# Performance work log

Measured on AMD Instinct MI355X. Metric: run time of the kernel, lower is better.

The kernel has to match this reference:

```python
import jax, jax.numpy as jnp
import numpy as np

DIM, H, K, RADIUS = 128, 4, 32, 0.3
DH = DIM // H
N, M = 16384, 4096


def setup_inputs() -> dict:
    key = jax.random.key(0)
    ks = jax.random.split(key, 16)
    s = 0.02
    return {
        "xyz": jax.random.normal(ks[0], (N, 3), jnp.float32),
        "feats": jax.random.normal(ks[1], (N, DIM), jnp.float32),
        "idx_center": jax.random.randint(ks[2], (M,), 0, N, jnp.int64),
        "Wq": jax.random.normal(ks[3], (DIM, DIM), jnp.float32) * s,
        "Wk": jax.random.normal(ks[4], (DIM, DIM), jnp.float32) * s,
        "Wv": jax.random.normal(ks[5], (DIM, DIM), jnp.float32) * s,
        "Wo": jax.random.normal(ks[6], (DIM, DIM), jnp.float32) * s,
        "bo": jnp.zeros((DIM,), jnp.float32),
        "g1": jnp.ones((DIM,), jnp.float32),
        "be1": jnp.zeros((DIM,), jnp.float32),
        "g2": jnp.ones((DIM,), jnp.float32),
        "be2": jnp.zeros((DIM,), jnp.float32),
        "W1": jax.random.normal(ks[7], (4 * DIM, DIM), jnp.float32) * s,
        "b1f": jnp.zeros((4 * DIM,), jnp.float32),
        "W2": jax.random.normal(ks[8], (DIM, 4 * DIM), jnp.float32) * s,
        "b2f": jnp.zeros((DIM,), jnp.float32),
    }


def _layernorm(x, g, b, eps=1e-5):
    mu = x.mean(-1, keepdims=True)
    var = ((x - mu) ** 2).mean(-1, keepdims=True)
    return (x - mu) / jnp.sqrt(var + eps) * g + b


def reference(xyz, feats, idx_center, Wq, Wk, Wv, Wo, bo, g1, be1, g2, be2, W1, b1f, W2, b2f):
    m = idx_center.shape[0]
    c_xyz = xyz[idx_center]          # (M,3)
    c_feat = feats[idx_center]       # (M,DIM)
    # pairwise Euclidean distance (M,N), like torch.cdist
    d2 = (jnp.sum(c_xyz * c_xyz, -1)[:, None] + jnp.sum(xyz * xyz, -1)[None, :]
          - 2.0 * (c_xyz @ xyz.T))
    dist = jnp.sqrt(jnp.maximum(d2, 1e-12))
    mask = dist < RADIUS
    mask = mask.at[jnp.arange(m), idx_center].set(True)  # force self-inclusion
    dmask = jnp.where(mask, dist, jnp.inf)
    neg_d, nbr_idx = jax.lax.top_k(-dmask, K)            # k smallest distances
    nbr_dist = -neg_d
    valid = jnp.isfinite(nbr_dist)                       # (M,K)
    nbr_feats = jnp.where(valid[..., None], feats[nbr_idx], 0.0)  # (M,K,DIM)
    # tiny per-center attention
    q = (c_feat @ Wq.T).reshape(m, H, DH)
    k = (nbr_feats @ Wk.T).reshape(m, K, H, DH).transpose(0, 2, 1, 3)  # (M,H,K,DH)
    v = (nbr_feats @ Wv.T).reshape(m, K, H, DH).transpose(0, 2, 1, 3)
    attn = jnp.einsum('mhd,mhkd->mhk', q * (DH ** -0.5), k)
    attn = jnp.where(valid[:, None, :], attn, -1e9)
    attn = jax.nn.softmax(attn, axis=-1)
    out = jnp.einsum('mhk,mhkd->mhd', attn, v)
    out = out.transpose(0, 2, 1).reshape(m, DIM)  # matches torch transpose(1,2).reshape
    upd = out @ Wo.T + bo
    c_feat = c_feat + _layernorm(upd, g1, be1)
    ffn = jax.nn.relu(c_feat @ W1.T + b1f) @ W2.T + b2f
    c_feat = c_feat + _layernorm(ffn, g2, be2)
    nearest = jnp.argmin(dist, axis=0)            # (N,) nearest center per point
    return feats + c_feat[nearest]
```

## Files before the change

kernel.cpp:

```cpp
#include <hip/hip_runtime.h>
#include <hip/hip_bf16.h>

#define DIMF 128
#define KNBR 32
#define NH 4
#define DH 32
#define RADIUS 0.3f
#define CB 8
#define CAND 256
#define PPB 32

#define PACK_BLOCKS 172

typedef unsigned long long u64t;
typedef _Float16 f16x8 __attribute__((ext_vector_type(8)));
typedef _Float16 f16x4 __attribute__((ext_vector_type(4)));
typedef float f32x4 __attribute__((ext_vector_type(4)));

__device__ __forceinline__ void tr4_tile(const float4* __restrict__ in4, float4* __restrict__ out4,
                                         int AI, int BI, int a0, int b0, int t, char* smem) {
    float4(*tile)[33] = (float4(*)[33])smem;
    int tx = t & 31, ty = t >> 5;
    for (int r = ty; r < 32; r += 8) tile[r][tx] = in4[(long)(b0 + r) * AI + a0 + tx];
    __syncthreads();
    for (int r = ty; r < 32; r += 8) out4[(long)(a0 + r) * BI + b0 + tx] = tile[tx][r];
}

__global__ __launch_bounds__(256) void pack_kernel(
    const float* __restrict__ xyz, const int* __restrict__ idxc,
    const float* __restrict__ Wq, const float* __restrict__ Wv,
    const float* __restrict__ Wo, const float* __restrict__ W1,
    const float* __restrict__ W2, const float* __restrict__ Wk,
    float4* __restrict__ qp4, float4* __restrict__ vp4, float4* __restrict__ op4,
    float4* __restrict__ kp4, f16x8* __restrict__ w1h, f16x8* __restrict__ w2h,
    float4* __restrict__ xyz4, float4* __restrict__ cds4, int N, int M) {
    __shared__ __align__(16) char smem[16896];
    int pk = blockIdx.x, t = threadIdx.x;
    if (pk < 4) {
        tr4_tile((const float4*)Wq, qp4, 32, 128, 0, pk * 32, t, smem);
    } else if (pk < 8) {
        tr4_tile((const float4*)Wv, vp4, 32, 128, 0, (pk - 4) * 32, t, smem);
    } else if (pk < 12) {
        tr4_tile((const float4*)Wo, op4, 32, 128, 0, (pk - 8) * 32, t, smem);
    } else if (pk < 28) {
        int idx = (pk - 12) * 256 + t;
        int q = idx >> 7, j = idx & 127;
        float4 w;
        w.x = Wk[(long)(4 * q + 0) * DIMF + j];
        w.y = Wk[(long)(4 * q + 1) * DIMF + j];
        w.z = Wk[(long)(4 * q + 2) * DIMF + j];
        w.w = Wk[(long)(4 * q + 3) * DIMF + j];
        kp4[q * DIMF + j] = w;
    } else if (pk < 92) {
        int idx = (pk - 28) * 256 + t;
        if (idx < N) {
            float x = xyz[3 * idx], y = xyz[3 * idx + 1], z = xyz[3 * idx + 2];
            xyz4[idx] = make_float4(x, y, z, (x * x + y * y) + z * z);
        }
    } else if (pk < 108) {
        int idx = (pk - 92) * 256 + t;
        if (idx < M) {
            int ic = idxc[idx];
            float cx = xyz[3 * ic], cy = xyz[3 * ic + 1], cz = xyz[3 * ic + 2];
            cds4[idx] = make_float4(-2.0f * cx, -2.0f * cy, -2.0f * cz,
                                    (cx * cx + cy * cy) + cz * cz);
        }
    } else if (pk < 140) {
        int e = (pk - 108) * 256 + t;
        int l = e & 63, ks = (e >> 6) & 3, nt = e >> 8;
        int row = nt * 16 + (l & 15);
        int cb = ks * 32 + (l >> 4) * 8;
        const float* src = W1 + (long)row * DIMF + cb;
        f16x8 v;
#pragma unroll
        for (int j = 0; j < 8; ++j) v[j] = (_Float16)src[j];
        w1h[e] = v;
    } else {
        int e = (pk - 140) * 256 + t;
        int l = e & 63, ks = (e >> 6) & 15, nt = e >> 10;
        int row = nt * 16 + (l & 15);
        int cb = ks * 32 + (l >> 4) * 8;
        const float* src = W2 + (long)row * (4 * DIMF) + cb;
        f16x8 v;
#pragma unroll
        for (int j = 0; j < 8; ++j) v[j] = (_Float16)src[j];
        w2h[e] = v;
    }
}

__global__ __launch_bounds__(256) void main_kernel(
    const float4* __restrict__ xyz4, const float4* __restrict__ cds4g,
    const float* __restrict__ feats, const int* __restrict__ idxc,
    const float4* __restrict__ qp4, const float4* __restrict__ kp4,
    const float4* __restrict__ vp4, const float4* __restrict__ op4,
    const float* __restrict__ bo, const float* __restrict__ g1,
    const float* __restrict__ be1, const float* __restrict__ g2,
    const float* __restrict__ be2, const f16x8* __restrict__ w1h,
    const float* __restrict__ b1f, const f16x8* __restrict__ w2h,
    const float* __restrict__ b2f, float* __restrict__ cfin,
    int* __restrict__ bestm, int N, int M) {
    __shared__ __align__(16) char smem[32768];
    __shared__ int nbrl[CB][KNBR];
    __shared__ int cnt[CB];

    int t = threadIdx.x;
    int b = blockIdx.x;
    int nAttn = M / CB;

    if (b >= nAttn) {
        float4* cds = (float4*)smem;
        int pt = t >> 3, q = t & 7;
        int n = (b - nAttn) * PPB + pt;
        float4 p4 = xyz4[n];
        float px = p4.x, py = p4.y, pz = p4.z;
        float bd0 = INFINITY, bd1 = INFINITY;
        int bm0 = 0, bm1 = 0;
        for (int c0 = 0; c0 < M; c0 += 1024) {
            __syncthreads();
            for (int i = t; i < 1024; i += 256) cds[i] = cds4g[c0 + i];
            __syncthreads();
#pragma unroll 8
            for (int i = 0; i < 64; ++i) {
                int ci0 = q + (2 * i) * 8, ci1 = q + (2 * i + 1) * 8;
                float4 ca = cds[ci0];
                float4 cb = cds[ci1];
                float sa = fmaf(ca.x, px, fmaf(ca.y, py, fmaf(ca.z, pz, ca.w)));
                float sb = fmaf(cb.x, px, fmaf(cb.y, py, fmaf(cb.z, pz, cb.w)));
                if (sa < bd0) { bd0 = sa; bm0 = c0 + ci0; }
                if (sb < bd1) { bd1 = sb; bm1 = c0 + ci1; }
            }
        }
        if (bd1 < bd0 || (bd1 == bd0 && bm1 < bm0)) { bd0 = bd1; bm0 = bm1; }
#pragma unroll
        for (int o = 1; o < 8; o <<= 1) {
            float obd = __shfl_xor(bd0, o);
            int obm = __shfl_xor(bm0, o);
            if (obd < bd0 || (obd == bd0 && obm < bm0)) { bd0 = obd; bm0 = obm; }
        }
        if (q == 0) bestm[n] = bm0;
        return;
    }

    int m0 = b * CB;

    {
        u64t(*cand)[CAND] = (u64t(*)[CAND])smem;
        if (t < CB) cnt[t] = 0;
        __syncthreads();
        float nx[CB], ny[CB], nz[CB], cw[CB];
#pragma unroll
        for (int tc = 0; tc < CB; ++tc) {
            float4 c4v = cds4g[m0 + tc];
            nx[tc] = c4v.x; ny[tc] = c4v.y; nz[tc] = c4v.z; cw[tc] = c4v.w;
        }
        const float R2 = RADIUS * RADIUS;
        for (int n = t; n < N; n += 256) {
            float4 p4 = xyz4[n];
            float rhs = R2 - p4.w;
#pragma unroll
            for (int tc = 0; tc < CB; ++tc) {
                float s = fmaf(nx[tc], p4.x, fmaf(ny[tc], p4.y, fmaf(nz[tc], p4.z, cw[tc])));
                if (s < rhs) {
                    int pos = atomicAdd(&cnt[tc], 1);
                    if (pos < CAND)
                        cand[tc][pos] = (((u64t)__float_as_uint(fmaxf(s + p4.w, 0.0f))) << 32) | (unsigned)n;
                }
            }
        }
        __syncthreads();
        int w = t >> 6, lane = t & 63;
        for (int rep = 0; rep < 2; ++rep) {
            int cidx = w + rep * 4;
            int C = cnt[cidx] < CAND ? cnt[cidx] : CAND;
            const u64t* vc = cand[cidx];
            if (C <= 64) {
                u64t mykey = (lane < C) ? vc[lane] : ~0ull;
                int rank = 0;
                for (int j = 0; j < C; ++j) rank += (vc[j] < mykey) ? 1 : 0;
                if (lane < C && rank < KNBR) nbrl[cidx][rank] = (int)(mykey & 0xffffffffu);
                if (lane >= C && lane < KNBR) nbrl[cidx][lane] = -1;
            } else {
                u64t mykey[4];
                int myrank[4];
#pragma unroll
                for (int s = 0; s < 4; ++s) {
                    int i = s * 64 + lane;
                    mykey[s] = (i < C) ? vc[i] : ~0ull;
                    myrank[s] = 0;
                }
                for (int j = 0; j < C; ++j) {
                    u64t kj = vc[j];
#pragma unroll
                    for (int s = 0; s < 4; ++s) myrank[s] += (kj < mykey[s]) ? 1 : 0;
                }
#pragma unroll
                for (int s = 0; s < 4; ++s) {
                    int i = s * 64 + lane;
                    if (i < C && myrank[s] < KNBR) nbrl[cidx][myrank[s]] = (int)(mykey[s] & 0xffffffffu);
                }
            }
        }
    }
    __syncthreads();

    float(*cf)[DIMF] = (float(*)[DIMF])smem;
    float(*cf2)[DIMF] = (float(*)[DIMF])(smem + 4096);
    float(*S1)[4 * DIMF] = (float(*)[4 * DIMF])(smem + 8192);
    float(*S2)[DIMF] = (float(*)[DIMF])(smem + 24576);
    float(*S3)[DIMF] = (float(*)[DIMF])(smem + 28672);

    int lane127 = t & 127;
    int cg = (t >> 7) * 4;
    int c8 = t >> 5, k32 = t & 31;

    {
        int ic = idxc[m0 + c8];
        *(float4*)&cf[c8][k32 * 4] = *(const float4*)&feats[(long)ic * DIMF + k32 * 4];
    }
    __syncthreads();

    {
        float acc[4] = {0.f, 0.f, 0.f, 0.f};
        for (int jj = 0; jj < 32; ++jj) {
            float4 w = qp4[jj * DIMF + lane127];
#pragma unroll
            for (int cc = 0; cc < 4; ++cc) {
                float4 x = *(const float4*)&cf[cg + cc][jj * 4];
                acc[cc] += w.x * x.x + w.y * x.y + w.z * x.z + w.w * x.w;
            }
        }
#pragma unroll
        for (int cc = 0; cc < 4; ++cc) S2[cg + cc][lane127] = acc[cc] * 0.17677669529663687f;
    }
    __syncthreads();

    {
        int j = lane127, hs = t >> 7;
#pragma unroll
        for (int hh = 0; hh < 2; ++hh) {
            int h = hs * 2 + hh;
            float acc[8] = {0.f, 0.f, 0.f, 0.f, 0.f, 0.f, 0.f, 0.f};
            for (int d4 = 0; d4 < 8; ++d4) {
                float4 w = kp4[(h * 8 + d4) * DIMF + j];
#pragma unroll
                for (int c = 0; c < 8; ++c) {
                    float4 qv = *(const float4*)&S2[c][h * DH + d4 * 4];
                    acc[c] += qv.x * w.x + qv.y * w.y + qv.z * w.z + qv.w * w.w;
                }
            }
#pragma unroll
            for (int c = 0; c < 8; ++c) S1[c][h * DIMF + j] = acc[c];
        }
    }
    __syncthreads();

    {
        int ni = nbrl[c8][k32];
        const float* nrow = feats + (long)(ni < 0 ? 0 : ni) * DIMF;
        float lg[4] = {0.f, 0.f, 0.f, 0.f};
        for (int jj = 0; jj < 32; ++jj) {
            float4 f = *(const float4*)&nrow[jj * 4];
#pragma unroll
            for (int h = 0; h < 4; ++h) {
                float4 qwv = *(const float4*)&S1[c8][h * DIMF + jj * 4];
                lg[h] += f.x * qwv.x + f.y * qwv.y + f.z * qwv.z + f.w * qwv.w;
            }
        }
        if (ni < 0) { lg[0] = -1e9f; lg[1] = -1e9f; lg[2] = -1e9f; lg[3] = -1e9f; }
#pragma unroll
        for (int h = 0; h < 4; ++h) {
            float mx = lg[h];
            for (int o = 16; o; o >>= 1) mx = fmaxf(mx, __shfl_xor(mx, o, 32));
            float e = expf(lg[h] - mx);
            float s = e;
            for (int o = 16; o; o >>= 1) s += __shfl_xor(s, o, 32);
            S3[c8][h * KNBR + k32] = e / s;
        }
    }
    __syncthreads();

    {
        int j4 = k32 * 4;
        float a0x = 0.f, a0y = 0.f, a0z = 0.f, a0w = 0.f;
        float a1x = 0.f, a1y = 0.f, a1z = 0.f, a1w = 0.f;
        float a2x = 0.f, a2y = 0.f, a2z = 0.f, a2w = 0.f;
        float a3x = 0.f, a3y = 0.f, a3z = 0.f, a3w = 0.f;
        for (int k = 0; k < KNBR; ++k) {
            int ni = nbrl[c8][k];
            const float* nrow = feats + (long)(ni < 0 ? 0 : ni) * DIMF;
            float4 f = *(const float4*)&nrow[j4];
            float w0 = S3[c8][0 * KNBR + k], w1 = S3[c8][1 * KNBR + k];
            float w2 = S3[c8][2 * KNBR + k], w3 = S3[c8][3 * KNBR + k];
            a0x += w0 * f.x; a0y += w0 * f.y; a0z += w0 * f.z; a0w += w0 * f.w;
            a1x += w1 * f.x; a1y += w1 * f.y; a1z += w1 * f.z; a1w += w1 * f.w;
            a2x += w2 * f.x; a2y += w2 * f.y; a2z += w2 * f.z; a2w += w2 * f.w;
            a3x += w3 * f.x; a3y += w3 * f.y; a3z += w3 * f.z; a3w += w3 * f.w;
        }
        __syncthreads();
        *(float4*)&S1[c8][0 * DIMF + j4] = make_float4(a0x, a0y, a0z, a0w);
        *(float4*)&S1[c8][1 * DIMF + j4] = make_float4(a1x, a1y, a1z, a1w);
        *(float4*)&S1[c8][2 * DIMF + j4] = make_float4(a2x, a2y, a2z, a2w);
        *(float4*)&S1[c8][3 * DIMF + j4] = make_float4(a3x, a3y, a3z, a3w);
    }
    __syncthreads();

    {
        int i = lane127, h = i >> 5, d = i & 31;
        float acc[4] = {0.f, 0.f, 0.f, 0.f};
        for (int jj = 0; jj < 32; ++jj) {
            float4 w = vp4[jj * DIMF + i];
#pragma unroll
            for (int cc = 0; cc < 4; ++cc) {
                float4 pv = *(const float4*)&S1[cg + cc][h * DIMF + jj * 4];
                acc[cc] += w.x * pv.x + w.y * pv.y + w.z * pv.z + w.w * pv.w;
            }
        }
        __syncthreads();
#pragma unroll
        for (int cc = 0; cc < 4; ++cc) S2[cg + cc][d * NH + h] = acc[cc];
    }
    __syncthreads();

    {
        int i = lane127;
        float acc[4] = {0.f, 0.f, 0.f, 0.f};
        for (int jj = 0; jj < 32; ++jj) {
            float4 w = op4[jj * DIMF + i];
#pragma unroll
            for (int cc = 0; cc < 4; ++cc) {
                float4 x = *(const float4*)&S2[cg + cc][jj * 4];
                acc[cc] += w.x * x.x + w.y * x.y + w.z * x.z + w.w * x.w;
            }
        }
        float b = bo[i];
        __syncthreads();
#pragma unroll
        for (int cc = 0; cc < 4; ++cc) S3[cg + cc][i] = acc[cc] + b;
    }
    __syncthreads();

    {
        int i4 = k32 * 4;
        float4 u = *(const float4*)&S3[c8][i4];
        float s = ((u.x + u.y) + u.z) + u.w;
        for (int o = 16; o; o >>= 1) s += __shfl_xor(s, o, 32);
        float mu = s * (1.0f / DIMF);
        float d0 = u.x - mu, d1 = u.y - mu, d2 = u.z - mu, d3 = u.w - mu;
        float vs = ((d0 * d0 + d1 * d1) + d2 * d2) + d3 * d3;
        for (int o = 16; o; o >>= 1) vs += __shfl_xor(vs, o, 32);
        float rs = 1.0f / sqrtf(vs * (1.0f / DIMF) + 1e-5f);
        float4 g = *(const float4*)&g1[i4];
        float4 b = *(const float4*)&be1[i4];
        float4 base = *(const float4*)&cf[c8][i4];
        float4 r;
        r.x = base.x + d0 * rs * g.x + b.x;
        r.y = base.y + d1 * rs * g.y + b.y;
        r.z = base.z + d2 * rs * g.z + b.z;
        r.w = base.w + d3 * rs * g.w + b.w;
        *(float4*)&cf2[c8][i4] = r;
        {
            int byteoff = (c8 * 256 + i4 * 2) ^ ((c8 & 7) << 4);
            f16x4 hv = {(_Float16)r.x, (_Float16)r.y, (_Float16)r.z, (_Float16)r.w};
            *(f16x4*)(smem + 24576 + byteoff) = hv;
        }
    }
    __syncthreads();

    {
        int lane = t & 63, w = t >> 6;
        int la = lane & 15, kg = lane >> 4;
        f16x8 afr[4];
#pragma unroll
        for (int ks = 0; ks < 4; ++ks) {
            int byteoff = (la * 256 + ks * 64 + kg * 16) ^ ((la & 7) << 4);
            afr[ks] = *(const f16x8*)(smem + 24576 + byteoff);
        }
#pragma unroll
        for (int nt0 = 0; nt0 < 8; ++nt0) {
            int nt = w * 8 + nt0;
            f32x4 acc = {0.f, 0.f, 0.f, 0.f};
#pragma unroll
            for (int ks = 0; ks < 4; ++ks) {
                f16x8 bfr = w1h[(nt * 4 + ks) * 64 + lane];
                acc = __builtin_amdgcn_mfma_f32_16x16x32_f16(afr[ks], bfr, acc, 0, 0, 0);
            }
            int col = nt * 16 + la;
            float bb = b1f[col];
#pragma unroll
            for (int r = 0; r < 4; ++r) {
                int row = kg * 4 + r;
                float v = fmaxf(acc[r] + bb, 0.f);
                int byteoff = (row * 1024 + col * 2) ^ ((row & 7) << 4);
                *(_Float16*)(smem + 8192 + byteoff) = (_Float16)v;
            }
        }
    }
    __syncthreads();

    {
        int lane = t & 63, w = t >> 6;
        int la = lane & 15, kg = lane >> 4;
        int nt0 = w * 2, nt1 = w * 2 + 1;
        f32x4 acc0 = {0.f, 0.f, 0.f, 0.f}, acc1 = {0.f, 0.f, 0.f, 0.f};
#pragma unroll
        for (int ks = 0; ks < 16; ++ks) {
            int byteoff = (la * 1024 + ks * 64 + kg * 16) ^ ((la & 7) << 4);
            f16x8 afr = *(const f16x8*)(smem + 8192 + byteoff);
            f16x8 b0 = w2h[(nt0 * 16 + ks) * 64 + lane];
            f16x8 b1v = w2h[(nt1 * 16 + ks) * 64 + lane];
            acc0 = __builtin_amdgcn_mfma_f32_16x16x32_f16(afr, b0, acc0, 0, 0, 0);
            acc1 = __builtin_amdgcn_mfma_f32_16x16x32_f16(afr, b1v, acc1, 0, 0, 0);
        }
        if (lane < 32) {
            float bb0 = b2f[nt0 * 16 + la];
            float bb1 = b2f[nt1 * 16 + la];
#pragma unroll
            for (int r = 0; r < 4; ++r) {
                int row = kg * 4 + r;
                S3[row][nt0 * 16 + la] = acc0[r] + bb0;
                S3[row][nt1 * 16 + la] = acc1[r] + bb1;
            }
        }
    }
    __syncthreads();

    {
        int i4 = k32 * 4;
        float4 u = *(const float4*)&S3[c8][i4];
        float s = ((u.x + u.y) + u.z) + u.w;
        for (int o = 16; o; o >>= 1) s += __shfl_xor(s, o, 32);
        float mu = s * (1.0f / DIMF);
        float d0 = u.x - mu, d1 = u.y - mu, d2 = u.z - mu, d3 = u.w - mu;
        float vs = ((d0 * d0 + d1 * d1) + d2 * d2) + d3 * d3;
        for (int o = 16; o; o >>= 1) vs += __shfl_xor(vs, o, 32);
        float rs = 1.0f / sqrtf(vs * (1.0f / DIMF) + 1e-5f);
        float4 g = *(const float4*)&g2[i4];
        float4 b = *(const float4*)&be2[i4];
        float4 base = *(const float4*)&cf2[c8][i4];
        float4 r;
        r.x = base.x + d0 * rs * g.x + b.x;
        r.y = base.y + d1 * rs * g.y + b.y;
        r.z = base.z + d2 * rs * g.z + b.z;
        r.w = base.w + d3 * rs * g.w + b.w;
        *(float4*)&cfin[(long)(m0 + c8) * DIMF + i4] = r;
    }
}

__global__ __launch_bounds__(256) void out_kernel(const float4* __restrict__ feats4,
                                                  const float* __restrict__ cfin,
                                                  const int* __restrict__ bestm,
                                                  float4* __restrict__ out4, int total) {
    int idx = blockIdx.x * 256 + threadIdx.x;
    if (idx >= total) return;
    int n = idx >> 5, c = idx & 31;
    const float4* cf4 = (const float4*)cfin;
    float4 f = feats4[idx];
    float4 g = cf4[(long)bestm[n] * 32 + c];
    out4[idx] = make_float4(f.x + g.x, f.y + g.y, f.z + g.z, f.w + g.w);
}

extern "C" void kernel_launch(void* const* d_in, const int* in_sizes, int n_in,
                              void* d_out, int out_size, void* d_ws, size_t ws_size,
                              hipStream_t stream) {
    const float* xyz = (const float*)d_in[0];
    const float* feats = (const float*)d_in[1];
    const int* idxc = (const int*)d_in[2];
    const float* Wq = (const float*)d_in[3];
    const float* Wk = (const float*)d_in[4];
    const float* Wv = (const float*)d_in[5];
    const float* Wo = (const float*)d_in[6];
    const float* bo = (const float*)d_in[7];
    const float* g1 = (const float*)d_in[8];
    const float* be1 = (const float*)d_in[9];
    const float* g2 = (const float*)d_in[10];
    const float* be2 = (const float*)d_in[11];
    const float* W1 = (const float*)d_in[12];
    const float* b1f = (const float*)d_in[13];
    const float* W2 = (const float*)d_in[14];
    const float* b2f = (const float*)d_in[15];

    int N = in_sizes[0] / 3;
    int M = in_sizes[2];

    char* ws = (char*)d_ws;
    size_t off = 0;
    float* cfin = (float*)(ws + off); off += (size_t)M * DIMF * 4;
    int* bestm = (int*)(ws + off); off += (size_t)N * 4;
    float4* qp4 = (float4*)(ws + off); off += (size_t)DIMF * DIMF * 4;
    float4* vp4 = (float4*)(ws + off); off += (size_t)DIMF * DIMF * 4;
    float4* op4 = (float4*)(ws + off); off += (size_t)DIMF * DIMF * 4;
    float4* kp4 = (float4*)(ws + off); off += (size_t)DIMF * DIMF * 4;
    f16x8* w1h = (f16x8*)(ws + off); off += (size_t)8192 * 16;
    f16x8* w2h = (f16x8*)(ws + off); off += (size_t)8192 * 16;
    float4* xyz4 = (float4*)(ws + off); off += (size_t)N * 16;
    float4* cds4 = (float4*)(ws + off); off += (size_t)M * 16;
    (void)ws_size; (void)n_in; (void)out_size;

    pack_kernel<<<PACK_BLOCKS, 256, 0, stream>>>(
        xyz, idxc, Wq, Wv, Wo, W1, W2, Wk,
        qp4, vp4, op4, kp4, w1h, w2h, xyz4, cds4, N, M);
    main_kernel<<<M / CB + N / PPB, 256, 0, stream>>>(
        xyz4, cds4, feats, idxc, qp4, kp4, vp4, op4, bo, g1, be1, g2, be2,
        w1h, b1f, w2h, b2f, cfin, bestm, N, M);
    out_kernel<<<(N * DIMF / 4 + 255) / 256, 256, 0, stream>>>(
        (const float4*)feats, cfin, bestm, (float4*)d_out, N * DIMF / 4);
}
```

Measured before the change: 167.9 us.

## Assign two centers per wavefront to remove block barriers in attention stages

Restructures the attention part of the main kernel so each 64-lane wavefront owns two centers end to end, with private shared-memory regions for q, q·Wk, softmax weights and the Wv/Wo stages. This removes most of the __syncthreads between the per-center stages. In exchange, each wave reloads the Wq/Wk/Wv/Wo weights itself, so global/L2 weight traffic grows up to fourfold per block. Shared memory grows from 32 KB to 52 KB, which may reduce occupancy.

```diff
diff --git a/kernel.cpp b/kernel.cpp
--- a/kernel.cpp
+++ b/kernel.cpp
@@ -99,7 +99,7 @@
     const float* __restrict__ b1f, const f16x8* __restrict__ w2h,
     const float* __restrict__ b2f, float* __restrict__ cfin,
     int* __restrict__ bestm, int N, int M) {
-    __shared__ __align__(16) char smem[32768];
+    __shared__ __align__(16) char smem[53248];
     __shared__ int nbrl[CB][KNBR];
     __shared__ int cnt[CB];
 
@@ -168,9 +168,9 @@
             }
         }
         __syncthreads();
-        int w = t >> 6, lane = t & 63;
+        int wv = t >> 6, lane = t & 63;
         for (int rep = 0; rep < 2; ++rep) {
-            int cidx = w + rep * 4;
+            int cidx = wv + rep * 4;
             int C = cnt[cidx] < CAND ? cnt[cidx] : CAND;
             const u64t* vc = cand[cidx];
             if (C <= 64) {
@@ -203,145 +203,139 @@
     }
     __syncthreads();
 
-    float(*cf)[DIMF] = (float(*)[DIMF])smem;
-    float(*cf2)[DIMF] = (float(*)[DIMF])(smem + 4096);
-    float(*S1)[4 * DIMF] = (float(*)[4 * DIMF])(smem + 8192);
-    float(*S2)[DIMF] = (float(*)[DIMF])(smem + 24576);
-    float(*S3)[DIMF] = (float(*)[DIMF])(smem + 28672);
-
-    int lane127 = t & 127;
-    int cg = (t >> 7) * 4;
-    int c8 = t >> 5, k32 = t & 31;
-
-    {
-        int ic = idxc[m0 + c8];
-        *(float4*)&cf[c8][k32 * 4] = *(const float4*)&feats[(long)ic * DIMF + k32 * 4];
-    }
-    __syncthreads();
-
-    {
-        float acc[4] = {0.f, 0.f, 0.f, 0.f};
+    int w = t >> 6, lane = t & 63;
+    float* qwp = (float*)(smem) + w * 1024;
+    float* cfw = (float*)(smem + 16384) + w * 256;
+    float* qb = (float*)(smem + 20480) + w * 256;
+    float* smu = (float*)(smem + 24576) + w * 256;
+    float* cf2w = (float*)(smem + 28672) + w * 256;
+    float* S3out = (float*)(smem + 16384);
+
+    int cl = lane >> 5, l31 = lane & 31;
+    int crow = 2 * w + cl;
+
+    {
+        int ic = idxc[m0 + crow];
+        *(float4*)(cfw + cl * 128 + l31 * 4) = *(const float4*)&feats[(long)ic * DIMF + l31 * 4];
+    }
+
+#pragma unroll
+    for (int c = 0; c < 2; ++c) {
+        float acc0 = 0.f, acc1 = 0.f;
+        const float4* cf4 = (const float4*)(cfw + c * 128);
         for (int jj = 0; jj < 32; ++jj) {
-            float4 w = qp4[jj * DIMF + lane127];
-#pragma unroll
-            for (int cc = 0; cc < 4; ++cc) {
-                float4 x = *(const float4*)&cf[cg + cc][jj * 4];
-                acc[cc] += w.x * x.x + w.y * x.y + w.z * x.z + w.w * x.w;
-            }
-        }
-#pragma unroll
-        for (int cc = 0; cc < 4; ++cc) S2[cg + cc][lane127] = acc[cc] * 0.17677669529663687f;
-    }
-    __syncthreads();
-
-    {
-        int j = lane127, hs = t >> 7;
-#pragma unroll
-        for (int hh = 0; hh < 2; ++hh) {
-            int h = hs * 2 + hh;
-            float acc[8] = {0.f, 0.f, 0.f, 0.f, 0.f, 0.f, 0.f, 0.f};
+            float4 x = cf4[jj];
+            float4 w0 = qp4[jj * DIMF + lane];
+            float4 w1 = qp4[jj * DIMF + lane + 64];
+            acc0 += w0.x * x.x + w0.y * x.y + w0.z * x.z + w0.w * x.w;
+            acc1 += w1.x * x.x + w1.y * x.y + w1.z * x.z + w1.w * x.w;
+        }
+        qb[c * 128 + lane] = acc0 * 0.17677669529663687f;
+        qb[c * 128 + lane + 64] = acc1 * 0.17677669529663687f;
+    }
+
+#pragma unroll
+    for (int c = 0; c < 2; ++c) {
+#pragma unroll
+        for (int h = 0; h < NH; ++h) {
+            float a0 = 0.f, a1 = 0.f;
+#pragma unroll
             for (int d4 = 0; d4 < 8; ++d4) {
-                float4 w = kp4[(h * 8 + d4) * DIMF + j];
-#pragma unroll
-                for (int c = 0; c < 8; ++c) {
-                    float4 qv = *(const float4*)&S2[c][h * DH + d4 * 4];
-                    acc[c] += qv.x * w.x + qv.y * w.y + qv.z * w.z + qv.w * w.w;
-                }
-            }
-#pragma unroll
-            for (int c = 0; c < 8; ++c) S1[c][h * DIMF + j] = acc[c];
-        }
-    }
-    __syncthreads();
-
-    {
-        int ni = nbrl[c8][k32];
+                float4 qv = *(const float4*)(qb + c * 128 + h * DH + d4 * 4);
+                float4 w0 = kp4[(h * 8 + d4) * DIMF + lane];
+                float4 w1 = kp4[(h * 8 + d4) * DIMF + lane + 64];
+                a0 += qv.x * w0.x + qv.y * w0.y + qv.z * w0.z + qv.w * w0.w;
+                a1 += qv.x * w1.x + qv.y * w1.y + qv.z * w1.z + qv.w * w1.w;
+            }
+            qwp[c * 512 + h * DIMF + lane] = a0;
+            qwp[c * 512 + h * DIMF + lane + 64] = a1;
+        }
+    }
+
+    {
+        int ni = nbrl[crow][l31];
         const float* nrow = feats + (long)(ni < 0 ? 0 : ni) * DIMF;
         float lg[4] = {0.f, 0.f, 0.f, 0.f};
+        const float4* qw4 = (const float4*)(qwp + cl * 512);
         for (int jj = 0; jj < 32; ++jj) {
             float4 f = *(const float4*)&nrow[jj * 4];
 #pragma unroll
-            for (int h = 0; h < 4; ++h) {
-                float4 qwv = *(const float4*)&S1[c8][h * DIMF + jj * 4];
-                lg[h] += f.x * qwv.x + f.y * qwv.y + f.z * qwv.z + f.w * qwv.w;
+            for (int h = 0; h < NH; ++h) {
+                float4 qv = qw4[h * 32 + jj];
+                lg[h] += f.x * qv.x + f.y * qv.y + f.z * qv.z + f.w * qv.w;
             }
         }
         if (ni < 0) { lg[0] = -1e9f; lg[1] = -1e9f; lg[2] = -1e9f; lg[3] = -1e9f; }
 #pragma unroll
-        for (int h = 0; h < 4; ++h) {
+        for (int h = 0; h < NH; ++h) {
             float mx = lg[h];
             for (int o = 16; o; o >>= 1) mx = fmaxf(mx, __shfl_xor(mx, o, 32));
             float e = expf(lg[h] - mx);
             float s = e;
             for (int o = 16; o; o >>= 1) s += __shfl_xor(s, o, 32);
-            S3[c8][h * KNBR + k32] = e / s;
-        }
-    }
-    __syncthreads();
-
-    {
-        int j4 = k32 * 4;
+            smu[cl * 128 + h * KNBR + l31] = e / s;
+        }
+    }
+
+    {
+        int j4 = l31 * 4;
         float a0x = 0.f, a0y = 0.f, a0z = 0.f, a0w = 0.f;
         float a1x = 0.f, a1y = 0.f, a1z = 0.f, a1w = 0.f;
         float a2x = 0.f, a2y = 0.f, a2z = 0.f, a2w = 0.f;
         float a3x = 0.f, a3y = 0.f, a3z = 0.f, a3w = 0.f;
         for (int k = 0; k < KNBR; ++k) {
-            int ni = nbrl[c8][k];
+            int ni = nbrl[crow][k];
             const float* nrow = feats + (long)(ni < 0 ? 0 : ni) * DIMF;
             float4 f = *(const float4*)&nrow[j4];
-            float w0 = S3[c8][0 * KNBR + k], w1 = S3[c8][1 * KNBR + k];
-            float w2 = S3[c8][2 * KNBR + k], w3 = S3[c8][3 * KNBR + k];
+            float w0 = smu[cl * 128 + 0 * KNBR + k], w1 = smu[cl * 128 + 1 * KNBR + k];
+            float w2 = smu[cl * 128 + 2 * KNBR + k], w3 = smu[cl * 128 + 3 * KNBR + k];
             a0x += w0 * f.x; a0y += w0 * f.y; a0z += w0 * f.z; a0w += w0 * f.w;
             a1x += w1 * f.x; a1y += w1 * f.y; a1z += w1 * f.z; a1w += w1 * f.w;
             a2x += w2 * f.x; a2y += w2 * f.y; a2z += w2 * f.z; a2w += w2 * f.w;
             a3x += w3 * f.x; a3y += w3 * f.y; a3z += w3 * f.z; a3w += w3 * f.w;
         }
-        __syncthreads();
-        *(float4*)&S1[c8][0 * DIMF + j4] = make_float4(a0x, a0y, a0z, a0w);
-        *(float4*)&S1[c8][1 * DIMF + j4] = make_float4(a1x, a1y, a1z, a1w);
-        *(float4*)&S1[c8][2 * DIMF + j4] = make_float4(a2x, a2y, a2z, a2w);
-        *(float4*)&S1[c8][3 * DIMF + j4] = make_float4(a3x, a3y, a3z, a3w);
-    }
-    __syncthreads();
-
-    {
-        int i = lane127, h = i >> 5, d = i & 31;
-        float acc[4] = {0.f, 0.f, 0.f, 0.f};
-        for (int jj = 0; jj < 32; ++jj) {
-            float4 w = vp4[jj * DIMF + i];
-#pragma unroll
-            for (int cc = 0; cc < 4; ++cc) {
-                float4 pv = *(const float4*)&S1[cg + cc][h * DIMF + jj * 4];
-                acc[cc] += w.x * pv.x + w.y * pv.y + w.z * pv.z + w.w * pv.w;
-            }
-        }
-        __syncthreads();
-#pragma unroll
-        for (int cc = 0; cc < 4; ++cc) S2[cg + cc][d * NH + h] = acc[cc];
-    }
-    __syncthreads();
-
-    {
-        int i = lane127;
-        float acc[4] = {0.f, 0.f, 0.f, 0.f};
-        for (int jj = 0; jj < 32; ++jj) {
-            float4 w = op4[jj * DIMF + i];
-#pragma unroll
-            for (int cc = 0; cc < 4; ++cc) {
-                float4 x = *(const float4*)&S2[cg + cc][jj * 4];
-                acc[cc] += w.x * x.x + w.y * x.y + w.z * x.z + w.w * x.w;
-            }
-        }
-        float b = bo[i];
-        __syncthreads();
-#pragma unroll
-        for (int cc = 0; cc < 4; ++cc) S3[cg + cc][i] = acc[cc] + b;
-    }
-    __syncthreads();
-
-    {
-        int i4 = k32 * 4;
-        float4 u = *(const float4*)&S3[c8][i4];
+        *(float4*)(qwp + cl * 512 + 0 * DIMF + j4) = make_float4(a0x, a0y, a0z, a0w);
+        *(float4*)(qwp + cl * 512 + 1 * DIMF + j4) = make_float4(a1x, a1y, a1z, a1w);
+        *(float4*)(qwp + cl * 512 + 2 * DIMF + j4) = make_float4(a2x, a2y, a2z, a2w);
+        *(float4*)(qwp + cl * 512 + 3 * DIMF + j4) = make_float4(a3x, a3y, a3z, a3w);
+    }
+
+#pragma unroll
+    for (int c = 0; c < 2; ++c) {
+#pragma unroll
+        for (int r = 0; r < 2; ++r) {
+            int i = lane + r * 64;
+            int h = i >> 5, d = i & 31;
+            float acc = 0.f;
+            const float4* p4 = (const float4*)(qwp + c * 512 + h * DIMF);
+            for (int jj = 0; jj < 32; ++jj) {
+                float4 wv = vp4[jj * DIMF + i];
+                float4 pv = p4[jj];
+                acc += wv.x * pv.x + wv.y * pv.y + wv.z * pv.z + wv.w * pv.w;
+            }
+            qb[c * 128 + d * NH + h] = acc;
+        }
+    }
+
+#pragma unroll
+    for (int c = 0; c < 2; ++c) {
+#pragma unroll
+        for (int r = 0; r < 2; ++r) {
+            int i = lane + r * 64;
+            float acc = 0.f;
+            const float4* u4 = (const float4*)(qb + c * 128);
+            for (int jj = 0; jj < 32; ++jj) {
+                float4 wv = op4[jj * DIMF + i];
+                float4 xv = u4[jj];
+                acc += wv.x * xv.x + wv.y * xv.y + wv.z * xv.z + wv.w * xv.w;
+            }
+            smu[c * 128 + i] = acc + bo[i];
+        }
+    }
+
+    {
+        int i4 = l31 * 4;
+        float4 u = *(const float4*)(smu + cl * 128 + i4);
         float s = ((u.x + u.y) + u.z) + u.w;
         for (int o = 16; o; o >>= 1) s += __shfl_xor(s, o, 32);
         float mu = s * (1.0f / DIMF);
@@ -350,30 +344,27 @@
         for (int o = 16; o; o >>= 1) vs += __shfl_xor(vs, o, 32);
         float rs = 1.0f / sqrtf(vs * (1.0f / DIMF) + 1e-5f);
         float4 g = *(const float4*)&g1[i4];
-        float4 b = *(const float4*)&be1[i4];
-        float4 base = *(const float4*)&cf[c8][i4];
+        float4 bb = *(const float4*)&be1[i4];
+        float4 base = *(const float4*)(cfw + cl * 128 + i4);
         float4 r;
-        r.x = base.x + d0 * rs * g.x + b.x;
-        r.y = base.y + d1 * rs * g.y + b.y;
-        r.z = base.z + d2 * rs * g.z + b.z;
-        r.w = base.w + d3 * rs * g.w + b.w;
-        *(float4*)&cf2[c8][i4] = r;
-        {
-            int byteoff = (c8 * 256 + i4 * 2) ^ ((c8 & 7) << 4);
-            f16x4 hv = {(_Float16)r.x, (_Float16)r.y, (_Float16)r.z, (_Float16)r.w};
-            *(f16x4*)(smem + 24576 + byteoff) = hv;
-        }
+        r.x = base.x + d0 * rs * g.x + bb.x;
+        r.y = base.y + d1 * rs * g.y + bb.y;
+        r.z = base.z + d2 * rs * g.z + bb.z;
+        r.w = base.w + d3 * rs * g.w + bb.w;
+        *(float4*)(cf2w + cl * 128 + i4) = r;
+        int byteoff = (crow * 256 + i4 * 2) ^ ((crow & 7) << 4);
+        f16x4 hv = {(_Float16)r.x, (_Float16)r.y, (_Float16)r.z, (_Float16)r.w};
+        *(f16x4*)(smem + 32768 + byteoff) = hv;
     }
     __syncthreads();
 
     {
-        int lane = t & 63, w = t >> 6;
         int la = lane & 15, kg = lane >> 4;
         f16x8 afr[4];
 #pragma unroll
         for (int ks = 0; ks < 4; ++ks) {
             int byteoff = (la * 256 + ks * 64 + kg * 16) ^ ((la & 7) << 4);
-            afr[ks] = *(const f16x8*)(smem + 24576 + byteoff);
+            afr[ks] = *(const f16x8*)(smem + 32768 + byteoff);
         }
 #pragma unroll
         for (int nt0 = 0; nt0 < 8; ++nt0) {
@@ -391,21 +382,20 @@
                 int row = kg * 4 + r;
                 float v = fmaxf(acc[r] + bb, 0.f);
                 int byteoff = (row * 1024 + col * 2) ^ ((row & 7) << 4);
-                *(_Float16*)(smem + 8192 + byteoff) = (_Float16)v;
+                *(_Float16*)(smem + 36864 + byteoff) = (_Float16)v;
             }
         }
     }
     __syncthreads();
 
     {
-        int lane = t & 63, w = t >> 6;
         int la = lane & 15, kg = lane >> 4;
         int nt0 = w * 2, nt1 = w * 2 + 1;
         f32x4 acc0 = {0.f, 0.f, 0.f, 0.f}, acc1 = {0.f, 0.f, 0.f, 0.f};
 #pragma unroll
         for (int ks = 0; ks < 16; ++ks) {
             int byteoff = (la * 1024 + ks * 64 + kg * 16) ^ ((la & 7) << 4);
-            f16x8 afr = *(const f16x8*)(smem + 8192 + byteoff);
+            f16x8 afr = *(const f16x8*)(smem + 36864 + byteoff);
             f16x8 b0 = w2h[(nt0 * 16 + ks) * 64 + lane];
             f16x8 b1v = w2h[(nt1 * 16 + ks) * 64 + lane];
             acc0 = __builtin_amdgcn_mfma_f32_16x16x32_f16(afr, b0, acc0, 0, 0, 0);
@@ -417,16 +407,16 @@
 #pragma unroll
             for (int r = 0; r < 4; ++r) {
                 int row = kg * 4 + r;
-                S3[row][nt0 * 16 + la] = acc0[r] + bb0;
-                S3[row][nt1 * 16 + la] = acc1[r] + bb1;
+                S3out[row * DIMF + nt0 * 16 + la] = acc0[r] + bb0;
+                S3out[row * DIMF + nt1 * 16 + la] = acc1[r] + bb1;
             }
         }
     }
     __syncthreads();
 
     {
-        int i4 = k32 * 4;
-        float4 u = *(const float4*)&S3[c8][i4];
+        int i4 = l31 * 4;
+        float4 u = *(const float4*)(S3out + crow * DIMF + i4);
         float s = ((u.x + u.y) + u.z) + u.w;
         for (int o = 16; o; o >>= 1) s += __shfl_xor(s, o, 32);
         float mu = s * (1.0f / DIMF);
@@ -435,14 +425,14 @@
         for (int o = 16; o; o >>= 1) vs += __shfl_xor(vs, o, 32);
         float rs = 1.0f / sqrtf(vs * (1.0f / DIMF) + 1e-5f);
         float4 g = *(const float4*)&g2[i4];
-        float4 b = *(const float4*)&be2[i4];
-        float4 base = *(const float4*)&cf2[c8][i4];
+        float4 bb = *(const float4*)&be2[i4];
+        float4 base = *(const float4*)(cf2w + cl * 128 + i4);
         float4 r;
-        r.x = base.x + d0 * rs * g.x + b.x;
-        r.y = base.y + d1 * rs * g.y + b.y;
-        r.z = base.z + d2 * rs * g.z + b.z;
-        r.w = base.w + d3 * rs * g.w + b.w;
-        *(float4*)&cfin[(long)(m0 + c8) * DIMF + i4] = r;
+        r.x = base.x + d0 * rs * g.x + bb.x;
+        r.y = base.y + d1 * rs * g.y + bb.y;
+        r.z = base.z + d2 * rs * g.z + bb.z;
+        r.w = base.w + d3 * rs * g.w + bb.w;
+        *(float4*)&cfin[(long)(m0 + crow) * DIMF + i4] = r;
     }
 }
 
```

New measurement: 343.3 us. +104.5%, slower.
